# Kernel optimization log

Measured on AMD Instinct MI355X. Metric: run time of the kernel, lower is better.

The kernel has to match this reference:

```python
import jax, jax.numpy as jnp
import numpy as np

N, F_IN, H, C, E = 100000, 128, 128, 40, 600000


def setup_inputs() -> dict:
    key = jax.random.key(0)
    ks = jax.random.split(key, 20)
    s = 0.05
    inp = {
        "x": jax.random.normal(ks[0], (N, F_IN), jnp.float32),
        "edge_index": jax.random.randint(ks[1], (2, E), 0, N, jnp.int64),
        "importance": jnp.ones((F_IN,), jnp.float32),
        "W1": jax.random.normal(ks[2], (H, F_IN), jnp.float32) * s,
        "bl1": jax.random.normal(ks[3], (H,), jnp.float32) * s,
        "bc1": jnp.zeros((H,), jnp.float32),
        "W2": jax.random.normal(ks[4], (H, H), jnp.float32) * s,
        "bl2": jax.random.normal(ks[5], (H,), jnp.float32) * s,
        "bc2": jnp.zeros((H,), jnp.float32),
        "W3": jax.random.normal(ks[6], (H, H), jnp.float32) * s,
        "bl3": jax.random.normal(ks[7], (H,), jnp.float32) * s,
        "bc3": jnp.zeros((H,), jnp.float32),
        "Wlin1": jax.random.normal(ks[8], (H, H), jnp.float32) * s,
        "blin1": jax.random.normal(ks[9], (H,), jnp.float32) * s,
        "Wlin2": jax.random.normal(ks[10], (C, H), jnp.float32) * s,
        "blin2": jax.random.normal(ks[11], (C,), jnp.float32) * s,
    }
    return inp


def balanced_conv(x, W, bl, bc, row, col):
    # lin, then symmetric-normalized message, mean-aggregated over targets
    n = x.shape[0]
    h = x @ W.T + bl                                   # [N, H]
    loops = jnp.arange(n)
    r = jnp.concatenate([row, loops])                  # sources (x_j index)
    c = jnp.concatenate([col, loops])                  # targets
    deg = jnp.zeros((n,), x.dtype).at[c].add(1.0)      # degree(col) incl. self-loops
    dinv = deg ** -0.5
    norm = dinv[r] * dinv[c]                           # [E+N]
    msg = norm[:, None] * h[r]                         # gather + scale
    agg = jnp.zeros((n, h.shape[1]), x.dtype).at[c].add(msg)  # scatter-add
    return agg / deg[:, None] + bc                     # mean aggr + bias


def reference(x, edge_index, importance, W1, bl1, bc1, W2, bl2, bc2,
              W3, bl3, bc3, Wlin1, blin1, Wlin2, blin2):
    row, col = edge_index[0], edge_index[1]
    h = x * importance
    h = jax.nn.relu(balanced_conv(h, W1, bl1, bc1, row, col))
    h = jax.nn.relu(balanced_conv(h, W2, bl2, bc2, row, col))
    h = jax.nn.relu(balanced_conv(h, W3, bl3, bc3, row, col))
    h = jax.nn.relu(h @ Wlin1.T + blin1)
    h = h @ Wlin2.T + blin2
    return jax.nn.log_softmax(h, axis=-1)
```

## Files before the change

### kernel.cpp

```cpp
#include <hip/hip_runtime.h>
#include <hip/hip_bf16.h>

#define F 128
#define C_CLS 40
#define NWSPLIT 35
#define ELLCAP 32
#define NBKT 9

typedef __attribute__((ext_vector_type(8))) short short8;
typedef __attribute__((ext_vector_type(4))) float float4v;
typedef unsigned short ushort;

__device__ inline float bf2f(ushort u) {
  unsigned int x = ((unsigned int)u) << 16;
  return __builtin_bit_cast(float, x);
}
__device__ inline ushort f2bf(float f) {
  __hip_bfloat16 h = __float2bfloat16(f);
  return __builtin_bit_cast(ushort, h);
}
__device__ inline void split_bf16(float f, ushort& hi, ushort& lo) {
  hi = f2bf(f);
  lo = f2bf(f - bf2f(hi));
}
__device__ inline int swz(int lane) { return lane ^ ((lane >> 4) & 3); }
__device__ inline int bucket_of(int cv) {
  int lim = cv < ELLCAP ? cv : ELLCAP;
  int nIt = (lim + 3) >> 2;
  return 8 - nIt;
}

__global__ __launch_bounds__(256) void setup_kernel(
    const float* __restrict__ W1, const float* __restrict__ imp,
    const float* __restrict__ W2, const float* __restrict__ W3,
    const float* __restrict__ Wl1, const float* __restrict__ Wh2,
    ushort* __restrict__ WhP,
    ushort* __restrict__ W2hH, ushort* __restrict__ W2lH,
    const int* __restrict__ row, const int* __restrict__ col,
    int* __restrict__ cnt, int* __restrict__ ell,
    int ne, int n) {
  int b = blockIdx.x;
  if (b < NWSPLIT) {
    int ci = b * 256 + threadIdx.x;
    if (ci < 8192) {
      const float* src[4] = {W1, W2, W3, Wl1};
      int p = ci >> 11, c = ci & 2047;
      int kc = c >> 10, ct = (c >> 7) & 7, ks = (c >> 6) & 1, ln = c & 63;
      int dl = swz(ln);
      int colw = ct * 16 + (dl & 15);
      int k = kc * 64 + ks * 32 + (dl >> 4) * 8;
      float4 f0 = *(const float4*)&src[p][(size_t)colw * F + k];
      float4 f1 = *(const float4*)&src[p][(size_t)colw * F + k + 4];
      float v[8] = {f0.x, f0.y, f0.z, f0.w, f1.x, f1.y, f1.z, f1.w};
      if (p == 0) {
        float4 i0 = *(const float4*)&imp[k];
        float4 i1 = *(const float4*)&imp[k + 4];
        v[0] *= i0.x; v[1] *= i0.y; v[2] *= i0.z; v[3] *= i0.w;
        v[4] *= i1.x; v[5] *= i1.y; v[6] *= i1.z; v[7] *= i1.w;
      }
      ushort hi[8];
#pragma unroll
      for (int j = 0; j < 8; ++j) hi[j] = f2bf(v[j]);
      *(short8*)&WhP[(size_t)ci * 8] = *(short8*)hi;
    } else if (ci < 8192 + 768) {
      int c = ci - 8192;
      int ct = c >> 8, ks = (c >> 6) & 3, ln = c & 63;
      int colw = ct * 16 + (ln & 15);
      int k = ks * 32 + (ln >> 4) * 8;
      float v[8];
      if (colw < C_CLS) {
        float4 f0 = *(const float4*)&Wh2[(size_t)colw * F + k];
        float4 f1 = *(const float4*)&Wh2[(size_t)colw * F + k + 4];
        v[0] = f0.x; v[1] = f0.y; v[2] = f0.z; v[3] = f0.w;
        v[4] = f1.x; v[5] = f1.y; v[6] = f1.z; v[7] = f1.w;
      } else {
#pragma unroll
        for (int j = 0; j < 8; ++j) v[j] = 0.f;
      }
      ushort hi[8], lo[8];
#pragma unroll
      for (int j = 0; j < 8; ++j) split_bf16(v[j], hi[j], lo[j]);
      *(short8*)&W2hH[(size_t)c * 8] = *(short8*)hi;
      *(short8*)&W2lH[(size_t)c * 8] = *(short8*)lo;
    }
  } else {
    int e = (b - NWSPLIT) * 256 + threadIdx.x;
    if (e < ne) {
      int r = row[e], c = col[e];
      int p = atomicAdd(&cnt[c], 1);
      if (p < ELLCAP) ell[(size_t)c * ELLCAP + p] = r;
    }
  }
}

__global__ __launch_bounds__(256) void prepass_kernel(
    const float* __restrict__ x, const int* __restrict__ cnt,
    int* __restrict__ ell, float* __restrict__ wsum, int* __restrict__ hist,
    ushort* __restrict__ Xs, ushort* __restrict__ Az,
    int n, int nbW, int nbX) {
  int b = blockIdx.x;
  if (b < nbW) {
    __shared__ int lh[NBKT];
    int t = threadIdx.x;
    if (t < NBKT) lh[t] = 0;
    __syncthreads();
    int node = b * 256 + t;
    if (node < n) {
      int cv = cnt[node];
      int lim = cv < ELLCAP ? cv : ELLCAP;
      int lim4 = (lim + 3) & ~3;
      float gs = 0.f;
      const int4* ep = (const int4*)&ell[(size_t)node * ELLCAP];
      for (int base = 0; base < lim; base += 4) {
        int4 rr = ep[base >> 2];
        bool p1 = base + 1 < lim, p2 = base + 2 < lim, p3 = base + 3 < lim;
        int r1 = p1 ? rr.y : rr.x;
        int r2 = p2 ? rr.z : rr.x;
        int r3 = p3 ? rr.w : rr.x;
        float g0 = rsqrtf((float)(cnt[rr.x] + 1));
        float g1 = p1 ? rsqrtf((float)(cnt[r1] + 1)) : 0.f;
        float g2 = p2 ? rsqrtf((float)(cnt[r2] + 1)) : 0.f;
        float g3 = p3 ? rsqrtf((float)(cnt[r3] + 1)) : 0.f;
        gs += (g0 + g1) + (g2 + g3);
      }
      float d = (float)(cv + 1);
      wsum[node] = rsqrtf(d) * gs + 1.0f / d;
      for (int p = lim; p < lim4; ++p) ell[(size_t)node * ELLCAP + p] = n;
      atomicAdd(&lh[bucket_of(cv)], 1);
    }
    __syncthreads();
    if (t < NBKT) atomicAdd(&hist[t], lh[t]);
  } else if (b < nbW + nbX) {
    size_t i = (size_t)(b - nbW) * 2048 + (size_t)threadIdx.x * 8;
    if (i < (size_t)n * F) {
      int node = (int)(i >> 7);
      float dc = rsqrtf((float)(cnt[node] + 1));
      float4 f0 = *(const float4*)&x[i];
      float4 f1 = *(const float4*)&x[i + 4];
      ushort o[8] = {f2bf(dc * f0.x), f2bf(dc * f0.y), f2bf(dc * f0.z), f2bf(dc * f0.w),
                     f2bf(dc * f1.x), f2bf(dc * f1.y), f2bf(dc * f1.z), f2bf(dc * f1.w)};
      *(short8*)&Xs[i] = *(short8*)o;
    }
  } else {
    int t = threadIdx.x;
    short8 z = (short8){0, 0, 0, 0, 0, 0, 0, 0};
    if (t < 16) *(short8*)&Xs[(size_t)n * F + t * 8] = z;
    else if (t < 32) *(short8*)&Az[(size_t)n * F + (t - 16) * 8] = z;
  }
}

__global__ __launch_bounds__(256) void perm_kernel(
    const int* __restrict__ cnt, const float* __restrict__ wsum,
    const int* __restrict__ hist, int* __restrict__ cursor,
    int* __restrict__ perm, int* __restrict__ cnt_s, float* __restrict__ wsum_s,
    const int* __restrict__ ell, int* __restrict__ ell_s, int n) {
  __shared__ int lh[NBKT], lbase[NBKT];
  int t = threadIdx.x;
  if (t < NBKT) lh[t] = 0;
  __syncthreads();
  int node = blockIdx.x * 256 + t;
  int bkt = 0, idx = 0, cv = 0;
  if (node < n) {
    cv = cnt[node];
    bkt = bucket_of(cv);
    idx = atomicAdd(&lh[bkt], 1);
  }
  __syncthreads();
  if (t < NBKT) {
    int pre = 0;
#pragma unroll
    for (int k = 0; k < NBKT; ++k)
      if (k < t) pre += hist[k];
    lbase[t] = pre + atomicAdd(&cursor[t], lh[t]);
  }
  __syncthreads();
  if (node < n) {
    int dst = lbase[bkt] + idx;
    perm[dst] = node;
    cnt_s[dst] = cv;
    wsum_s[dst] = wsum[node];
    const int4* src = (const int4*)&ell[(size_t)node * ELLCAP];
    int4* d = (int4*)&ell_s[(size_t)dst * ELLCAP];
#pragma unroll
    for (int k = 0; k < 8; ++k) d[k] = src[k];
  }
}

template <bool SCALE_OUT>
__global__ __launch_bounds__(256) void conv_fused(
    const int* __restrict__ cnt_s, const int* __restrict__ ell_s,
    const int* __restrict__ perm,
    const ushort* __restrict__ Xs, const ushort* __restrict__ Wh,
    const float* __restrict__ wsum_s, const float* __restrict__ bl,
    const float* __restrict__ bc, ushort* __restrict__ OUT, int n) {
  const int t = threadIdx.x;
  const int w = t >> 6, lane = t & 63, quad = lane >> 4, cl = lane & 15;
  const int gid = blockIdx.x * 64 + w * 16 + cl;
  const bool valid = gid < n;
  const int sgid = valid ? gid : 0;
  const int node = perm[sgid];

  float acc[4][8];
#pragma unroll
  for (int ks = 0; ks < 4; ++ks)
#pragma unroll
    for (int q = 0; q < 8; ++q) acc[ks][q] = 0.f;

  float dc = 1.f, id = 1.f;
  int nIt = 0;
  if (valid) {
    int cv = cnt_s[sgid];
    float d = (float)(cv + 1);
    dc = rsqrtf(d);
    id = 1.0f / d;
    int lim = cv < ELLCAP ? cv : ELLCAP;
    nIt = (lim + 3) >> 2;
  }
  const int4* ep = (const int4*)&ell_s[(size_t)sgid * ELLCAP];
  const int qoff = quad * 8;

  if (nIt > 0) {
    int4 rr = ep[0];
    for (int it = 0; it < nIt; ++it) {
      const ushort* r0 = &Xs[(size_t)rr.x * F + qoff];
      const ushort* r1 = &Xs[(size_t)rr.y * F + qoff];
      const ushort* r2 = &Xs[(size_t)rr.z * F + qoff];
      const ushort* r3 = &Xs[(size_t)rr.w * F + qoff];
      short8 v[4][4];
#pragma unroll
      for (int ks = 0; ks < 4; ++ks) {
        v[0][ks] = *(const short8*)&r0[ks * 32];
        v[1][ks] = *(const short8*)&r1[ks * 32];
        v[2][ks] = *(const short8*)&r2[ks * 32];
        v[3][ks] = *(const short8*)&r3[ks * 32];
      }
      int jn = (it + 1 < nIt) ? it + 1 : it;
      rr = ep[jn];
#pragma unroll
      for (int ks = 0; ks < 4; ++ks)
#pragma unroll
        for (int q = 0; q < 8; ++q) {
          float t0 = bf2f((ushort)v[0][ks][q]) + bf2f((ushort)v[1][ks][q]);
          float t1 = bf2f((ushort)v[2][ks][q]) + bf2f((ushort)v[3][ks][q]);
          acc[ks][q] += t0 + t1;
        }
    }
  }

  short8 sfrag[4];
  if (valid) {
    const ushort* sq = &Xs[(size_t)node * F + qoff];
#pragma unroll
    for (int ks = 0; ks < 4; ++ks) {
      short8 sv = *(const short8*)&sq[ks * 32];
      ushort o[8];
#pragma unroll
      for (int q = 0; q < 8; ++q)
        o[q] = f2bf(dc * (acc[ks][q] + bf2f((ushort)sv[q])));
      sfrag[ks] = *(short8*)o;
    }
  } else {
#pragma unroll
    for (int ks = 0; ks < 4; ++ks) sfrag[ks] = (short8){0, 0, 0, 0, 0, 0, 0, 0};
  }

  float4v co[8];
#pragma unroll
  for (int mt = 0; mt < 8; ++mt) co[mt] = (float4v){0.f, 0.f, 0.f, 0.f};
  const int sl = swz(lane);
#pragma unroll
  for (int ks = 0; ks < 4; ++ks) {
    const int base2 = ((ks >> 1) * 1024 + (ks & 1) * 64 + sl) * 8;
#pragma unroll
    for (int mt = 0; mt < 8; ++mt) {
      short8 a_h = *(const short8*)&Wh[base2 + mt * 1024];
      co[mt] = __builtin_amdgcn_mfma_f32_16x16x32_bf16(a_h, sfrag[ks], co[mt], 0, 0, 0);
    }
  }

  if (valid) {
    float ws = wsum_s[sgid];
#pragma unroll
    for (int mt = 0; mt < 8; ++mt) {
      float4 blv = *(const float4*)&bl[mt * 16 + quad * 4];
      float4 bcv = *(const float4*)&bc[mt * 16 + quad * 4];
      float v0 = fmaxf((co[mt][0] + ws * blv.x) * id + bcv.x, 0.f);
      float v1 = fmaxf((co[mt][1] + ws * blv.y) * id + bcv.y, 0.f);
      float v2 = fmaxf((co[mt][2] + ws * blv.z) * id + bcv.z, 0.f);
      float v3 = fmaxf((co[mt][3] + ws * blv.w) * id + bcv.w, 0.f);
      if (SCALE_OUT) { v0 *= dc; v1 *= dc; v2 *= dc; v3 *= dc; }
      ushort o[4] = {f2bf(v0), f2bf(v1), f2bf(v2), f2bf(v3)};
      *(ushort4*)&OUT[(size_t)node * F + mt * 16 + quad * 4] = *(ushort4*)o;
    }
  }
}

__global__ __launch_bounds__(256) void head_fused(const ushort* __restrict__ X,
    const ushort* __restrict__ Wl1h, const float* __restrict__ bl,
    const ushort* __restrict__ W2h, const ushort* __restrict__ W2l,
    const float* __restrict__ b2, float* __restrict__ out, int nrows) {
  __shared__ ushort sH[8192];
  __shared__ float b2s[48];
  const int t = threadIdx.x;
  if (t < 48) b2s[t] = (t < C_CLS) ? b2[t] : -1e30f;

  const int w = t >> 6, lane = t & 63;
  const int quad = lane >> 4, cl = lane & 15;
  const int sl = swz(lane);
  const int row0 = (blockIdx.x * 4 + w) * 16;
  char* sHb = (char*)sH;

  float4v acc1[8];
#pragma unroll
  for (int mt = 0; mt < 8; ++mt) acc1[mt] = (float4v){0.f, 0.f, 0.f, 0.f};
  const int gr1 = row0 + cl;
#pragma unroll
  for (int ks = 0; ks < 4; ++ks) {
    short8 b;
    if (gr1 < nrows) b = *(const short8*)&X[(size_t)gr1 * F + ks * 32 + quad * 8];
    else b = (short8){0, 0, 0, 0, 0, 0, 0, 0};
    const int base = ((ks >> 1) * 1024 + (ks & 1) * 64 + sl) * 8;
#pragma unroll
    for (int mt = 0; mt < 8; ++mt) {
      short8 a_h = *(const short8*)&Wl1h[base + mt * 1024];
      acc1[mt] = __builtin_amdgcn_mfma_f32_16x16x32_bf16(a_h, b, acc1[mt], 0, 0, 0);
    }
  }
#pragma unroll
  for (int mt = 0; mt < 8; ++mt) {
    float4 bv = *(const float4*)&bl[mt * 16 + quad * 4];
    ushort o[4];
    o[0] = f2bf(fmaxf(acc1[mt][0] + bv.x, 0.f));
    o[1] = f2bf(fmaxf(acc1[mt][1] + bv.y, 0.f));
    o[2] = f2bf(fmaxf(acc1[mt][2] + bv.z, 0.f));
    o[3] = f2bf(fmaxf(acc1[mt][3] + bv.w, 0.f));
    int ch = (mt * 2 + (quad >> 1)) ^ cl;
    *(ushort4*)&sHb[w * 4096 + cl * 256 + ch * 16 + (quad & 1) * 8] = *(ushort4*)o;
  }
  __syncthreads();

  float4v acc[3];
#pragma unroll
  for (int ct = 0; ct < 3; ++ct) acc[ct] = (float4v){0.f, 0.f, 0.f, 0.f};
#pragma unroll
  for (int ks = 0; ks < 4; ++ks) {
    int ch2 = (ks * 4 + quad) ^ cl;
    short8 a = *(short8*)&sHb[w * 4096 + cl * 256 + ch2 * 16];
#pragma unroll
    for (int ct = 0; ct < 3; ++ct) {
      int chunk = ((ct * 4 + ks) * 64 + lane) * 8;
      short8 b_h = *(const short8*)&W2h[chunk];
      short8 b_l = *(const short8*)&W2l[chunk];
      acc[ct] = __builtin_amdgcn_mfma_f32_16x16x32_bf16(a, b_h, acc[ct], 0, 0, 0);
      acc[ct] = __builtin_amdgcn_mfma_f32_16x16x32_bf16(a, b_l, acc[ct], 0, 0, 0);
    }
  }

  float b0 = b2s[cl], b1 = b2s[16 + cl], b2v = b2s[32 + cl];
  float lse[4];
#pragma unroll
  for (int reg = 0; reg < 4; ++reg) {
    float v0 = acc[0][reg] + b0;
    float v1 = acc[1][reg] + b1;
    float v2 = acc[2][reg] + b2v;
    acc[0][reg] = v0; acc[1][reg] = v1; acc[2][reg] = v2;
    float m = fmaxf(fmaxf(v0, v1), v2);
#pragma unroll
    for (int o = 1; o < 16; o <<= 1) m = fmaxf(m, __shfl_xor(m, o));
    float s = __expf(v0 - m) + __expf(v1 - m) + __expf(v2 - m);
#pragma unroll
    for (int o = 1; o < 16; o <<= 1) s += __shfl_xor(s, o);
    lse[reg] = logf(s) + m;
  }
#pragma unroll
  for (int reg = 0; reg < 4; ++reg) {
    int gr = row0 + quad * 4 + reg;
    if (gr < nrows) {
      out[(size_t)gr * C_CLS + cl] = acc[0][reg] - lse[reg];
      out[(size_t)gr * C_CLS + 16 + cl] = acc[1][reg] - lse[reg];
      if (cl < 8) out[(size_t)gr * C_CLS + 32 + cl] = acc[2][reg] - lse[reg];
    }
  }
}

extern "C" void kernel_launch(void* const* d_in, const int* in_sizes, int n_in,
                              void* d_out, int out_size, void* d_ws, size_t ws_size,
                              hipStream_t stream) {
  const float* x    = (const float*)d_in[0];
  const int*   ei   = (const int*)d_in[1];
  const float* imp  = (const float*)d_in[2];
  const float* W1   = (const float*)d_in[3];
  const float* bl1  = (const float*)d_in[4];
  const float* bc1  = (const float*)d_in[5];
  const float* W2   = (const float*)d_in[6];
  const float* bl2  = (const float*)d_in[7];
  const float* bc2  = (const float*)d_in[8];
  const float* W3   = (const float*)d_in[9];
  const float* bl3  = (const float*)d_in[10];
  const float* bc3  = (const float*)d_in[11];
  const float* Wl1  = (const float*)d_in[12];
  const float* bli1 = (const float*)d_in[13];
  const float* Wl2  = (const float*)d_in[14];
  const float* bli2 = (const float*)d_in[15];
  float* out = (float*)d_out;

  const int N = in_sizes[0] / F;
  const int E = in_sizes[1] / 2;

  ushort* A16 = (ushort*)d_ws;
  ushort* B16 = A16 + (size_t)(N + 1) * F;
  ushort* WhP = B16 + (size_t)(N + 1) * F;
  ushort* W2hH = WhP + 65536;
  ushort* W2lH = W2hH + 6144;
  float* wsum = (float*)(W2lH + 6144);
  float* wsum_s = wsum + N;
  int*   cnt  = (int*)(wsum_s + N);
  int*   hist = cnt + N;
  int*   cursor = hist + NBKT;
  int*   cnt_s = cursor + NBKT;
  int*   perm = cnt_s + N;
  int*   ell  = perm + N;
  int*   ell_s = ell + (size_t)32 * N;

  const int* rowv = ei;
  const int* colv = ei + E;

  int nbE  = (E + 255) / 256;
  int nbW  = (N + 255) / 256;
  int nbX  = (N * F + 2047) / 2048;
  int nbCv = (N + 63) / 64;
  int nbHd = (N + 63) / 64;

  hipMemsetAsync(cnt, 0, ((size_t)N + 2 * NBKT) * sizeof(int), stream);
  setup_kernel<<<NWSPLIT + nbE, 256, 0, stream>>>(
      W1, imp, W2, W3, Wl1, Wl2, WhP, W2hH, W2lH, rowv, colv, cnt, ell, E, N);
  prepass_kernel<<<nbW + nbX + 1, 256, 0, stream>>>(
      x, cnt, ell, wsum, hist, B16, A16, N, nbW, nbX);
  perm_kernel<<<nbW, 256, 0, stream>>>(cnt, wsum, hist, cursor,
                                       perm, cnt_s, wsum_s, ell, ell_s, N);

  conv_fused<true ><<<nbCv, 256, 0, stream>>>(cnt_s, ell_s, perm, B16, WhP,         wsum_s, bl1, bc1, A16, N);
  conv_fused<true ><<<nbCv, 256, 0, stream>>>(cnt_s, ell_s, perm, A16, WhP + 16384, wsum_s, bl2, bc2, B16, N);
  conv_fused<false><<<nbCv, 256, 0, stream>>>(cnt_s, ell_s, perm, B16, WhP + 32768, wsum_s, bl3, bc3, A16, N);

  head_fused<<<nbHd, 256, 0, stream>>>(A16, WhP + 49152, bli1, W2hH, W2lH, bli2, out, N);
}
```

Before: 338.8 us.

## Split conv into chunked-layout gather kernel and separate GEMM kernel

```diff
diff --git a/kernel.cpp b/kernel.cpp
--- a/kernel.cpp
+++ b/kernel.cpp
@@ -29,6 +29,7 @@
   int nIt = (lim + 3) >> 2;
   return 8 - nIt;
 }
+
 
 __global__ __launch_bounds__(256) void setup_kernel(
     const float* __restrict__ W1, const float* __restrict__ imp,
@@ -98,6 +99,7 @@
     int* __restrict__ ell, float* __restrict__ wsum, int* __restrict__ hist,
     ushort* __restrict__ Xs, ushort* __restrict__ Az,
     int n, int nbW, int nbX) {
+  const size_t CS = (size_t)(n + 1) * 16;
   int b = blockIdx.x;
   if (b < nbW) {
     __shared__ int lh[NBKT];
@@ -134,25 +136,27 @@
     size_t i = (size_t)(b - nbW) * 2048 + (size_t)threadIdx.x * 8;
     if (i < (size_t)n * F) {
       int node = (int)(i >> 7);
+      int f0 = (int)(i & 127);
       float dc = rsqrtf((float)(cnt[node] + 1));
-      float4 f0 = *(const float4*)&x[i];
-      float4 f1 = *(const float4*)&x[i + 4];
-      ushort o[8] = {f2bf(dc * f0.x), f2bf(dc * f0.y), f2bf(dc * f0.z), f2bf(dc * f0.w),
-                     f2bf(dc * f1.x), f2bf(dc * f1.y), f2bf(dc * f1.z), f2bf(dc * f1.w)};
-      *(short8*)&Xs[i] = *(short8*)o;
+      float4 v0 = *(const float4*)&x[i];
+      float4 v1 = *(const float4*)&x[i + 4];
+      ushort o[8] = {f2bf(dc * v0.x), f2bf(dc * v0.y), f2bf(dc * v0.z), f2bf(dc * v0.w),
+                     f2bf(dc * v1.x), f2bf(dc * v1.y), f2bf(dc * v1.z), f2bf(dc * v1.w)};
+      *(short8*)&Xs[(size_t)(f0 >> 4) * CS + (size_t)node * 16 + (f0 & 15)] = *(short8*)o;
     }
   } else {
     int t = threadIdx.x;
     short8 z = (short8){0, 0, 0, 0, 0, 0, 0, 0};
-    if (t < 16) *(short8*)&Xs[(size_t)n * F + t * 8] = z;
-    else if (t < 32) *(short8*)&Az[(size_t)n * F + (t - 16) * 8] = z;
+    if (t < 16)
+      *(short8*)&Xs[(size_t)(t >> 1) * CS + (size_t)n * 16 + (t & 1) * 8] = z;
+    else if (t < 32)
+      *(short8*)&Az[(size_t)((t - 16) >> 1) * CS + (size_t)n * 16 + ((t - 16) & 1) * 8] = z;
   }
 }
 
 __global__ __launch_bounds__(256) void perm_kernel(
-    const int* __restrict__ cnt, const float* __restrict__ wsum,
-    const int* __restrict__ hist, int* __restrict__ cursor,
-    int* __restrict__ perm, int* __restrict__ cnt_s, float* __restrict__ wsum_s,
+    const int* __restrict__ cnt, const int* __restrict__ hist,
+    int* __restrict__ cursor, int* __restrict__ perm, int* __restrict__ cnt_s,
     const int* __restrict__ ell, int* __restrict__ ell_s, int n) {
   __shared__ int lh[NBKT], lbase[NBKT];
   int t = threadIdx.x;
@@ -178,7 +182,6 @@
     int dst = lbase[bkt] + idx;
     perm[dst] = node;
     cnt_s[dst] = cv;
-    wsum_s[dst] = wsum[node];
     const int4* src = (const int4*)&ell[(size_t)node * ELLCAP];
     int4* d = (int4*)&ell_s[(size_t)dst * ELLCAP];
 #pragma unroll
@@ -186,82 +189,77 @@
   }
 }
 
-template <bool SCALE_OUT>
-__global__ __launch_bounds__(256) void conv_fused(
+__global__ __launch_bounds__(256) void gather_chunk(
     const int* __restrict__ cnt_s, const int* __restrict__ ell_s,
     const int* __restrict__ perm,
-    const ushort* __restrict__ Xs, const ushort* __restrict__ Wh,
-    const float* __restrict__ wsum_s, const float* __restrict__ bl,
-    const float* __restrict__ bc, ushort* __restrict__ OUT, int n) {
+    const ushort* __restrict__ Xc, ushort* __restrict__ Sc, int n) {
+  const size_t CS = (size_t)(n + 1) * 16;
+  int k = blockIdx.x & 7;
+  int grp = blockIdx.x >> 3;
+  int tp = threadIdx.x >> 1;
+  int half = (threadIdx.x & 1) * 8;
+  int gid = grp * 128 + tp;
+  if (gid >= n) return;
+  int node = perm[gid];
+  int cv = cnt_s[gid];
+  float dc = rsqrtf((float)(cv + 1));
+  int lim = cv < ELLCAP ? cv : ELLCAP;
+  int nIt = (lim + 3) >> 2;
+  const int4* ep = (const int4*)&ell_s[(size_t)gid * ELLCAP];
+  const ushort* base = Xc + k * CS + half;
+
+  float acc[8] = {0, 0, 0, 0, 0, 0, 0, 0};
+  for (int it = 0; it < nIt; ++it) {
+    int4 rr = ep[it];
+    short8 v0 = *(const short8*)&base[(size_t)rr.x * 16];
+    short8 v1 = *(const short8*)&base[(size_t)rr.y * 16];
+    short8 v2 = *(const short8*)&base[(size_t)rr.z * 16];
+    short8 v3 = *(const short8*)&base[(size_t)rr.w * 16];
+#pragma unroll
+    for (int q = 0; q < 8; ++q) {
+      float t0 = bf2f((ushort)v0[q]) + bf2f((ushort)v1[q]);
+      float t1 = bf2f((ushort)v2[q]) + bf2f((ushort)v3[q]);
+      acc[q] += t0 + t1;
+    }
+  }
+  short8 sv = *(const short8*)&base[(size_t)node * 16];
+  ushort o[8];
+#pragma unroll
+  for (int q = 0; q < 8; ++q)
+    o[q] = f2bf(dc * (acc[q] + bf2f((ushort)sv[q])));
+  *(short8*)&Sc[k * CS + (size_t)node * 16 + half] = *(short8*)o;
+}
+
+template <bool SCALE_OUT>
+__global__ __launch_bounds__(256) void gemm_mid(
+    const ushort* __restrict__ S, const ushort* __restrict__ Wh,
+    const int* __restrict__ cnt, const float* __restrict__ wsum,
+    const float* __restrict__ bl, const float* __restrict__ bc,
+    ushort* __restrict__ OUT, int n) {
+  __shared__ ushort sWh[16384];
+  const size_t CS = (size_t)(n + 1) * 16;
   const int t = threadIdx.x;
+#pragma unroll
+  for (int pp = 0; pp < 8; ++pp) {
+    int ci = t + pp * 256;
+    *(short8*)&sWh[ci * 8] = *(const short8*)&Wh[(size_t)ci * 8];
+  }
+  __syncthreads();
+
   const int w = t >> 6, lane = t & 63, quad = lane >> 4, cl = lane & 15;
-  const int gid = blockIdx.x * 64 + w * 16 + cl;
-  const bool valid = gid < n;
-  const int sgid = valid ? gid : 0;
-  const int node = perm[sgid];
-
-  float acc[4][8];
-#pragma unroll
-  for (int ks = 0; ks < 4; ++ks)
-#pragma unroll
-    for (int q = 0; q < 8; ++q) acc[ks][q] = 0.f;
-
-  float dc = 1.f, id = 1.f;
-  int nIt = 0;
+  const int gr = blockIdx.x * 64 + w * 16 + cl;
+  const bool valid = gr < n;
+
+  short8 b[4];
   if (valid) {
-    int cv = cnt_s[sgid];
-    float d = (float)(cv + 1);
-    dc = rsqrtf(d);
-    id = 1.0f / d;
-    int lim = cv < ELLCAP ? cv : ELLCAP;
-    nIt = (lim + 3) >> 2;
-  }
-  const int4* ep = (const int4*)&ell_s[(size_t)sgid * ELLCAP];
-  const int qoff = quad * 8;
-
-  if (nIt > 0) {
-    int4 rr = ep[0];
-    for (int it = 0; it < nIt; ++it) {
-      const ushort* r0 = &Xs[(size_t)rr.x * F + qoff];
-      const ushort* r1 = &Xs[(size_t)rr.y * F + qoff];
-      const ushort* r2 = &Xs[(size_t)rr.z * F + qoff];
-      const ushort* r3 = &Xs[(size_t)rr.w * F + qoff];
-      short8 v[4][4];
-#pragma unroll
-      for (int ks = 0; ks < 4; ++ks) {
-        v[0][ks] = *(const short8*)&r0[ks * 32];
-        v[1][ks] = *(const short8*)&r1[ks * 32];
-        v[2][ks] = *(const short8*)&r2[ks * 32];
-        v[3][ks] = *(const short8*)&r3[ks * 32];
-      }
-      int jn = (it + 1 < nIt) ? it + 1 : it;
-      rr = ep[jn];
-#pragma unroll
-      for (int ks = 0; ks < 4; ++ks)
-#pragma unroll
-        for (int q = 0; q < 8; ++q) {
-          float t0 = bf2f((ushort)v[0][ks][q]) + bf2f((ushort)v[1][ks][q]);
-          float t1 = bf2f((ushort)v[2][ks][q]) + bf2f((ushort)v[3][ks][q]);
-          acc[ks][q] += t0 + t1;
-        }
-    }
-  }
-
-  short8 sfrag[4];
-  if (valid) {
-    const ushort* sq = &Xs[(size_t)node * F + qoff];
 #pragma unroll
     for (int ks = 0; ks < 4; ++ks) {
-      short8 sv = *(const short8*)&sq[ks * 32];
-      ushort o[8];
-#pragma unroll
-      for (int q = 0; q < 8; ++q)
-        o[q] = f2bf(dc * (acc[ks][q] + bf2f((ushort)sv[q])));
-      sfrag[ks] = *(short8*)o;
+      int c = 2 * ks + (quad >> 1), off = (quad & 1) * 8;
+      b[ks] = *(const short8*)&S[c * CS + (size_t)gr * 16 + off];
     }
   } else {
 #pragma unroll
-    for (int ks = 0; ks < 4; ++ks) sfrag[ks] = (short8){0, 0, 0, 0, 0, 0, 0, 0};
+    for (int ks = 0; ks < 4; ++ks) b[ks] = (short8){0, 0, 0, 0, 0, 0, 0, 0};
   }
 
   float4v co[8];
@@ -273,13 +271,16 @@
     const int base2 = ((ks >> 1) * 1024 + (ks & 1) * 64 + sl) * 8;
 #pragma unroll
     for (int mt = 0; mt < 8; ++mt) {
-      short8 a_h = *(const short8*)&Wh[base2 + mt * 1024];
-      co[mt] = __builtin_amdgcn_mfma_f32_16x16x32_bf16(a_h, sfrag[ks], co[mt], 0, 0, 0);
+      short8 a_h = *(short8*)&sWh[base2 + mt * 1024];
+      co[mt] = __builtin_amdgcn_mfma_f32_16x16x32_bf16(a_h, b[ks], co[mt], 0, 0, 0);
     }
   }
 
   if (valid) {
-    float ws = wsum_s[sgid];
+    float d = (float)(cnt[gr] + 1);
+    float dc = rsqrtf(d);
+    float id = 1.0f / d;
+    float ws = wsum[gr];
 #pragma unroll
     for (int mt = 0; mt < 8; ++mt) {
       float4 blv = *(const float4*)&bl[mt * 16 + quad * 4];
@@ -290,7 +291,7 @@
       float v3 = fmaxf((co[mt][3] + ws * blv.w) * id + bcv.w, 0.f);
       if (SCALE_OUT) { v0 *= dc; v1 *= dc; v2 *= dc; v3 *= dc; }
       ushort o[4] = {f2bf(v0), f2bf(v1), f2bf(v2), f2bf(v3)};
-      *(ushort4*)&OUT[(size_t)node * F + mt * 16 + quad * 4] = *(ushort4*)o;
+      *(ushort4*)&OUT[mt * CS + (size_t)gr * 16 + quad * 4] = *(ushort4*)o;
     }
   }
 }
@@ -301,6 +302,7 @@
     const float* __restrict__ b2, float* __restrict__ out, int nrows) {
   __shared__ ushort sH[8192];
   __shared__ float b2s[48];
+  const size_t CS = (size_t)(nrows + 1) * 16;
   const int t = threadIdx.x;
   if (t < 48) b2s[t] = (t < C_CLS) ? b2[t] : -1e30f;
 
@@ -317,8 +319,12 @@
 #pragma unroll
   for (int ks = 0; ks < 4; ++ks) {
     short8 b;
-    if (gr1 < nrows) b = *(const short8*)&X[(size_t)gr1 * F + ks * 32 + quad * 8];
-    else b = (short8){0, 0, 0, 0, 0, 0, 0, 0};
+    if (gr1 < nrows) {
+      int c = 2 * ks + (quad >> 1), off = (quad & 1) * 8;
+      b = *(const short8*)&X[c * CS + (size_t)gr1 * 16 + off];
+    } else {
+      b = (short8){0, 0, 0, 0, 0, 0, 0, 0};
+    }
     const int base = ((ks >> 1) * 1024 + (ks & 1) * 64 + sl) * 8;
 #pragma unroll
     for (int mt = 0; mt < 8; ++mt) {
@@ -413,8 +419,7 @@
   ushort* W2hH = WhP + 65536;
   ushort* W2lH = W2hH + 6144;
   float* wsum = (float*)(W2lH + 6144);
-  float* wsum_s = wsum + N;
-  int*   cnt  = (int*)(wsum_s + N);
+  int*   cnt  = (int*)(wsum + N);
   int*   hist = cnt + N;
   int*   cursor = hist + NBKT;
   int*   cnt_s = cursor + NBKT;
@@ -428,20 +433,24 @@
   int nbE  = (E + 255) / 256;
   int nbW  = (N + 255) / 256;
   int nbX  = (N * F + 2047) / 2048;
-  int nbCv = (N + 63) / 64;
-  int nbHd = (N + 63) / 64;
+  int nbGa = 8 * ((N + 127) / 128);
+  int nbGe = (N + 63) / 64;
 
   hipMemsetAsync(cnt, 0, ((size_t)N + 2 * NBKT) * sizeof(int), stream);
   setup_kernel<<<NWSPLIT + nbE, 256, 0, stream>>>(
       W1, imp, W2, W3, Wl1, Wl2, WhP, W2hH, W2lH, rowv, colv, cnt, ell, E, N);
   prepass_kernel<<<nbW + nbX + 1, 256, 0, stream>>>(
       x, cnt, ell, wsum, hist, B16, A16, N, nbW, nbX);
-  perm_kernel<<<nbW, 256, 0, stream>>>(cnt, wsum, hist, cursor,
-                                       perm, cnt_s, wsum_s, ell, ell_s, N);
-
-  conv_fused<true ><<<nbCv, 256, 0, stream>>>(cnt_s, ell_s, perm, B16, WhP,         wsum_s, bl1, bc1, A16, N);
-  conv_fused<true ><<<nbCv, 256, 0, stream>>>(cnt_s, ell_s, perm, A16, WhP + 16384, wsum_s, bl2, bc2, B16, N);
-  conv_fused<false><<<nbCv, 256, 0, stream>>>(cnt_s, ell_s, perm, B16, WhP + 32768, wsum_s, bl3, bc3, A16, N);
-
-  head_fused<<<nbHd, 256, 0, stream>>>(A16, WhP + 49152, bli1, W2hH, W2lH, bli2, out, N);
-}
+  perm_kernel<<<nbW, 256, 0, stream>>>(cnt, hist, cursor, perm, cnt_s, ell, ell_s, N);
+
+  gather_chunk<<<nbGa, 256, 0, stream>>>(cnt_s, ell_s, perm, B16, A16, N);
+  gemm_mid<true ><<<nbGe, 256, 0, stream>>>(A16, WhP, cnt, wsum, bl1, bc1, B16, N);
+
+  gather_chunk<<<nbGa, 256, 0, stream>>>(cnt_s, ell_s, perm, B16, A16, N);
+  gemm_mid<true ><<<nbGe, 256, 0, stream>>>(A16, WhP + 16384, cnt, wsum, bl2, bc2, B16, N);
+
+  gather_chunk<<<nbGa, 256, 0, stream>>>(cnt_s, ell_s, perm, B16, A16, N);
+  gemm_mid<false><<<nbGe, 256, 0, stream>>>(A16, WhP + 32768, cnt, wsum, bl3, bc3, B16, N);
+
+  head_fused<<<nbGe, 256, 0, stream>>>(B16, WhP + 49152, bli1, W2hH, W2lH, bli2, out, N);
+}
```

New measurement: 396.1 us. 1.17x slower.
